# Kernel optimization log

Hardware: AMD Instinct MI355X
Metric: run time of the kernel (lower is better)

Reference implementation:

```python
import jax, jax.numpy as jnp
import numpy as np

KW = 31       # avg_pool kernel
PAD = 15      # padding (count_include_pad=True => divide by KW*KW always)


def _box_avg(x):
    # F.avg_pool2d(x, 31, stride=1, padding=15) with count_include_pad=True
    s = jax.lax.reduce_window(
        x, 0.0, jax.lax.add,
        window_dimensions=(1, 1, KW, KW),
        window_strides=(1, 1, 1, 1),
        padding=((0, 0), (0, 0), (PAD, PAD), (PAD, PAD)))
    return s / (KW * KW)


def setup_inputs() -> dict:
    key = jax.random.key(0)
    k1, k2 = jax.random.split(key)
    B, C, H, W = 64, 1, 512, 512
    pred = jax.random.normal(k1, (B, C, H, W), dtype=jnp.float32)
    mask = jax.random.uniform(k2, (B, C, H, W), dtype=jnp.float32)
    return {"pred": pred, "mask": mask}


def reference(pred, mask):
    weit = 1.0 + 5.0 * jnp.abs(_box_avg(mask) - mask)
    # stable BCE-with-logits, elementwise
    bce = jnp.maximum(pred, 0.0) - pred * mask + jnp.log1p(jnp.exp(-jnp.abs(pred)))
    # NOTE: original passes reduce='none' which PyTorch's legacy handling maps to
    # reduction='mean' -> wbce is a global scalar; the weit normalization cancels.
    wbce = bce.mean()  # scalar, broadcast over [B, C]
    p = jax.nn.sigmoid(pred)
    inter = (p * mask * weit).sum(axis=(2, 3))          # [B, C]
    union = ((p + mask) * weit).sum(axis=(2, 3))        # [B, C]
    wiou = 1.0 - (inter + 1.0) / (union - inter + 1.0)  # [B, C]
    return (wbce + wiou).mean()
```

## Files before the change

### kernel.cpp

```cpp
#include <hip/hip_runtime.h>
#include <math.h>

#define BDIM 64
#define HDIM 512
#define WDIM 512
#define KW   31
#define PAD  15
#define INV_KK (1.0f / 961.0f)
#define TH   32
#define NPIX ((size_t)BDIM * HDIM * WDIM)

#define NACC 129

__global__ void zero_acc_kernel(double* acc) {
    int i = threadIdx.x;
    if (i < NACC) acc[i] = 0.0;
}

template<int CTRL, int RMASK>
__device__ __forceinline__ float dpp_add(float p) {
    int t = __builtin_amdgcn_update_dpp(0, __builtin_bit_cast(int, p),
                                        CTRL, RMASK, 0xf, true);
    return p + __builtin_bit_cast(float, t);
}

__device__ __forceinline__ float wave_iscan(float p) {
    p = dpp_add<0x111, 0xf>(p);
    p = dpp_add<0x112, 0xf>(p);
    p = dpp_add<0x114, 0xf>(p);
    p = dpp_add<0x118, 0xf>(p);
    p = dpp_add<0x142, 0xa>(p);
    p = dpp_add<0x143, 0xc>(p);
    return p;
}

__device__ __forceinline__ float wave_iscan30(float p) {
    p = dpp_add<0x111, 0xf>(p);
    p = dpp_add<0x112, 0xf>(p);
    p = dpp_add<0x114, 0xf>(p);
    p = dpp_add<0x118, 0xf>(p);
    p = dpp_add<0x142, 0xa>(p);
    return p;
}

__device__ __forceinline__ float wave_shr1(float p) {
    int t = __builtin_amdgcn_update_dpp(0, __builtin_bit_cast(int, p),
                                        0x138 , 0xf, 0xf, true);
    return __builtin_bit_cast(float, t);
}

__global__ __launch_bounds__(512, 6)
void fused_kernel(const float* __restrict__ pred,
                  const float* __restrict__ mask,
                  double* __restrict__ acc) {
    __shared__ float red[3][8];

    const int b    = blockIdx.x;
    const int y0   = blockIdx.y * TH;
    const int x    = threadIdx.x;
    const int lane = x & 63;
    const int wv   = x >> 6;
    const int s    = wv * 64;

    const float* mbase = mask + (size_t)b * HDIM * WDIM;
    const float* pbase = pred + (size_t)b * HDIM * WDIM;

    const int acol = s - 15 + lane;
    const int bcol = s + 49 + lane;
    const bool a_ok = (acol >= 0) && (acol < WDIM);
    const bool b_ok = (lane < 30) && (bcol < WDIM);

    const int tstart = y0 - PAD;
    const int tend   = y0 + TH - 1 + PAD;
    const int smax   = (tstart > 0) ? tstart : 0;

    float vsA = 0.f, vsB = 0.f;
    float bce_acc = 0.f, inter_acc = 0.f, uni_acc = 0.f;

    auto load_halo = [&](int row, float& A, float& B) {
        A = 0.f; B = 0.f;
        if (row >= 0 && row < HDIM) {
            const float* rp = mbase + (size_t)row * WDIM;
            if (a_ok) A = rp[acol];
            if (b_ok) B = rp[bcol];
        }
    };
    auto load_sub = [&](int row, float& A, float& B) {
        A = 0.f; B = 0.f;
        if (row >= smax) {
            const float* rp = mbase + (size_t)row * WDIM;
            if (a_ok) A = rp[acol];
            if (b_ok) B = rp[bcol];
        }
    };
    auto load_emit = [&](int row, float& M, float& P) {
        M = 0.f; P = 0.f;
        if (row <= tend) {
            const size_t off = (size_t)(row - PAD) * WDIM + x;
            M = mbase[off];
            P = pbase[off];
        }
    };

    auto process = [&](float A, float B, float S, float T, float M, float P) {
        vsA += A - S;
        vsB += B - T;
        float pa = wave_iscan(vsA);
        float pb = wave_iscan30(vsB);
        const float atot = __builtin_bit_cast(float,
            __builtin_amdgcn_readlane(__builtin_bit_cast(int, pa), 63));
        const float v1 = __shfl(pa, (lane + 30) & 63);
        const float v2 = __shfl(pb, (lane + 30) & 63);
        const float Phi = (lane <= 33) ? v1 : (atot + v2);
        const float Plo = wave_shr1(pa);
        const float hs  = Phi - Plo;

        const float box  = hs * INV_KK;
        const float weit = 1.f + 5.f * fabsf(box - M);
        const float e1   = __expf(-fabsf(P));
        const float bce  = fmaxf(P, 0.f) - P * M + __logf(1.f + e1);
        const float rr   = __builtin_amdgcn_rcpf(1.f + e1);
        const float sp   = (P >= 0.f) ? rr : e1 * rr;
        bce_acc   += bce;
        inter_acc += sp * M * weit;
        uni_acc   += (sp + M) * weit;
    };

    float cA[2], cB[2];
    load_halo(tstart,     cA[0], cB[0]);
    load_halo(tstart + 1, cA[1], cB[1]);
    for (int t = tstart; t < y0 + PAD; t += 2) {
        float nA[2], nB[2];
        load_halo(t + 2, nA[0], nB[0]);
        load_halo(t + 3, nA[1], nB[1]);
        vsA += cA[0] + cA[1];
        vsB += cB[0] + cB[1];
        cA[0] = nA[0]; cA[1] = nA[1]; cB[0] = nB[0]; cB[1] = nB[1];
    }

    float cS[2], cT[2], cM[2], cP[2];
    load_sub(y0 - 16, cS[0], cT[0]);
    load_sub(y0 - 15, cS[1], cT[1]);
    load_emit(y0 + PAD,     cM[0], cP[0]);
    load_emit(y0 + PAD + 1, cM[1], cP[1]);

    for (int t = y0 + PAD; t <= tend; t += 2) {
        float nA[2], nB[2], nS[2], nT[2], nM[2], nP[2];
        load_halo(t + 2, nA[0], nB[0]);
        load_halo(t + 3, nA[1], nB[1]);
        load_sub (t - 29, nS[0], nT[0]);
        load_sub (t - 28, nS[1], nT[1]);
        load_emit(t + 2, nM[0], nP[0]);
        load_emit(t + 3, nM[1], nP[1]);

        process(cA[0], cB[0], cS[0], cT[0], cM[0], cP[0]);
        process(cA[1], cB[1], cS[1], cT[1], cM[1], cP[1]);

        cA[0] = nA[0]; cA[1] = nA[1]; cB[0] = nB[0]; cB[1] = nB[1];
        cS[0] = nS[0]; cS[1] = nS[1]; cT[0] = nT[0]; cT[1] = nT[1];
        cM[0] = nM[0]; cM[1] = nM[1]; cP[0] = nP[0]; cP[1] = nP[1];
    }

#pragma unroll
    for (int off = 32; off > 0; off >>= 1) {
        bce_acc   += __shfl_down(bce_acc, off);
        inter_acc += __shfl_down(inter_acc, off);
        uni_acc   += __shfl_down(uni_acc, off);
    }
    if (lane == 0) {
        red[0][wv] = bce_acc;
        red[1][wv] = inter_acc;
        red[2][wv] = uni_acc;
    }
    __syncthreads();
    if (threadIdx.x == 0) {
        float bs = 0.f, is = 0.f, us = 0.f;
#pragma unroll
        for (int w = 0; w < 8; ++w) { bs += red[0][w]; is += red[1][w]; us += red[2][w]; }
        atomicAdd(&acc[0],      (double)bs);
        atomicAdd(&acc[1 + b],  (double)is);
        atomicAdd(&acc[65 + b], (double)us);
    }
}

__global__ void finalize_kernel(const double* __restrict__ acc, float* __restrict__ out) {
    const int b = threadIdx.x;
    double inter = acc[1 + b];
    double uni   = acc[65 + b];
    double wiou  = 1.0 - (inter + 1.0) / (uni - inter + 1.0);
#pragma unroll
    for (int off = 32; off > 0; off >>= 1) wiou += __shfl_down(wiou, off);
    if (b == 0) {
        double wbce = acc[0] / (double)NPIX;
        out[0] = (float)(wbce + wiou / (double)BDIM);
    }
}

extern "C" void kernel_launch(void* const* d_in, const int* in_sizes, int n_in,
                              void* d_out, int out_size, void* d_ws, size_t ws_size,
                              hipStream_t stream) {
    const float* pred = (const float*)d_in[0];
    const float* mask = (const float*)d_in[1];
    float* out = (float*)d_out;
    double* acc = (double*)d_ws;

    zero_acc_kernel<<<1, 256, 0, stream>>>(acc);

    dim3 grid(BDIM, HDIM / TH);
    fused_kernel<<<grid, WDIM, 0, stream>>>(pred, mask, acc);

    finalize_kernel<<<1, 64, 0, stream>>>(acc, out);
}
```

Before: 169.1 us.

## Deepen load prefetch to two row pairs with clamped branchless loads and full unroll

Result: slower. 183.9 us (+8.7%).

```diff
diff --git a/kernel.cpp b/kernel.cpp
--- a/kernel.cpp
+++ b/kernel.cpp
@@ -49,7 +49,7 @@
     return __builtin_bit_cast(float, t);
 }
 
-__global__ __launch_bounds__(512, 6)
+__global__ __launch_bounds__(512, 8)
 void fused_kernel(const float* __restrict__ pred,
                   const float* __restrict__ mask,
                   double* __restrict__ acc) {
@@ -67,8 +67,10 @@
 
     const int acol = s - 15 + lane;
     const int bcol = s + 49 + lane;
-    const bool a_ok = (acol >= 0) && (acol < WDIM);
-    const bool b_ok = (lane < 30) && (bcol < WDIM);
+    const int acolc = (acol < 0) ? 0 : ((acol > WDIM - 1) ? WDIM - 1 : acol);
+    const int bcolc = (bcol > WDIM - 1) ? WDIM - 1 : bcol;
+    const float aMul = (acol >= 0 && acol < WDIM) ? 1.f : 0.f;
+    const float bMul = (lane < 30 && bcol < WDIM) ? 1.f : 0.f;
 
     const int tstart = y0 - PAD;
     const int tend   = y0 + TH - 1 + PAD;
@@ -77,36 +79,35 @@
     float vsA = 0.f, vsB = 0.f;
     float bce_acc = 0.f, inter_acc = 0.f, uni_acc = 0.f;
 
-    auto load_halo = [&](int row, float& A, float& B) {
-        A = 0.f; B = 0.f;
-        if (row >= 0 && row < HDIM) {
-            const float* rp = mbase + (size_t)row * WDIM;
-            if (a_ok) A = rp[acol];
-            if (b_ok) B = rp[bcol];
-        }
-    };
-    auto load_sub = [&](int row, float& A, float& B) {
-        A = 0.f; B = 0.f;
-        if (row >= smax) {
-            const float* rp = mbase + (size_t)row * WDIM;
-            if (a_ok) A = rp[acol];
-            if (b_ok) B = rp[bcol];
-        }
-    };
-    auto load_emit = [&](int row, float& M, float& P) {
-        M = 0.f; P = 0.f;
-        if (row <= tend) {
-            const size_t off = (size_t)(row - PAD) * WDIM + x;
-            M = mbase[off];
-            P = pbase[off];
-        }
+    auto ld_halo = [&](int row, float& A, float& B) {
+        int rc = row;
+        if (rc < 0) rc = 0;
+        if (rc > HDIM - 1) rc = HDIM - 1;
+        const float* rp = mbase + (size_t)rc * WDIM;
+        A = rp[acolc];
+        B = rp[bcolc];
+        if (row < 0 || row >= HDIM) { A = 0.f; B = 0.f; }
+    };
+    auto ld_sub = [&](int row, float& S, float& T) {
+        int rc = (row < smax) ? smax : row;
+        const float* rp = mbase + (size_t)rc * WDIM;
+        S = rp[acolc];
+        T = rp[bcolc];
+        if (row < smax) { S = 0.f; T = 0.f; }
+    };
+    auto ld_emit = [&](int row, float& M, float& P) {
+        int rc = row - PAD;
+        if (rc > HDIM - 1) rc = HDIM - 1;
+        const size_t off = (size_t)rc * WDIM + x;
+        M = mbase[off];
+        P = pbase[off];
     };
 
     auto process = [&](float A, float B, float S, float T, float M, float P) {
         vsA += A - S;
         vsB += B - T;
-        float pa = wave_iscan(vsA);
-        float pb = wave_iscan30(vsB);
+        float pa = wave_iscan(vsA * aMul);
+        float pb = wave_iscan30(vsB * bMul);
         const float atot = __builtin_bit_cast(float,
             __builtin_amdgcn_readlane(__builtin_bit_cast(int, pa), 63));
         const float v1 = __shfl(pa, (lane + 30) & 63);
@@ -126,39 +127,63 @@
         uni_acc   += (sp + M) * weit;
     };
 
-    float cA[2], cB[2];
-    load_halo(tstart,     cA[0], cB[0]);
-    load_halo(tstart + 1, cA[1], cB[1]);
-    for (int t = tstart; t < y0 + PAD; t += 2) {
-        float nA[2], nB[2];
-        load_halo(t + 2, nA[0], nB[0]);
-        load_halo(t + 3, nA[1], nB[1]);
-        vsA += cA[0] + cA[1];
-        vsB += cB[0] + cB[1];
-        cA[0] = nA[0]; cA[1] = nA[1]; cB[0] = nB[0]; cB[1] = nB[1];
-    }
-
-    float cS[2], cT[2], cM[2], cP[2];
-    load_sub(y0 - 16, cS[0], cT[0]);
-    load_sub(y0 - 15, cS[1], cT[1]);
-    load_emit(y0 + PAD,     cM[0], cP[0]);
-    load_emit(y0 + PAD + 1, cM[1], cP[1]);
-
-    for (int t = y0 + PAD; t <= tend; t += 2) {
-        float nA[2], nB[2], nS[2], nT[2], nM[2], nP[2];
-        load_halo(t + 2, nA[0], nB[0]);
-        load_halo(t + 3, nA[1], nB[1]);
-        load_sub (t - 29, nS[0], nT[0]);
-        load_sub (t - 28, nS[1], nT[1]);
-        load_emit(t + 2, nM[0], nP[0]);
-        load_emit(t + 3, nM[1], nP[1]);
-
-        process(cA[0], cB[0], cS[0], cT[0], cM[0], cP[0]);
-        process(cA[1], cB[1], cS[1], cT[1], cM[1], cP[1]);
-
-        cA[0] = nA[0]; cA[1] = nA[1]; cB[0] = nB[0]; cB[1] = nB[1];
-        cS[0] = nS[0]; cS[1] = nS[1]; cT[0] = nT[0]; cT[1] = nT[1];
-        cM[0] = nM[0]; cM[1] = nM[1]; cP[0] = nP[0]; cP[1] = nP[1];
+    const int t0 = y0 + PAD;
+
+    float wA0, wB0, wA1, wB1;
+    float xA0, xB0, xA1, xB1;
+    ld_halo(tstart,     wA0, wB0);
+    ld_halo(tstart + 1, wA1, wB1);
+    ld_halo(tstart + 2, xA0, xB0);
+    ld_halo(tstart + 3, xA1, xB1);
+
+    float qS0, qT0, qS1, qT1, rS0, rT0, rS1, rT1;
+    float qM0, qP0, qM1, qP1, rM0, rP0, rM1, rP1;
+    ld_sub (t0 - 31, qS0, qT0);
+    ld_sub (t0 - 30, qS1, qT1);
+    ld_sub (t0 - 29, rS0, rT0);
+    ld_sub (t0 - 28, rS1, rT1);
+    ld_emit(t0,      qM0, qP0);
+    ld_emit(t0 + 1,  qM1, qP1);
+    ld_emit(t0 + 2,  rM0, rP0);
+    ld_emit(t0 + 3,  rM1, rP1);
+
+#pragma unroll
+    for (int i = 0; i < 15; ++i) {
+        const int t = tstart + 2 * i;
+        float nA0, nB0, nA1, nB1;
+        ld_halo(t + 4, nA0, nB0);
+        ld_halo(t + 5, nA1, nB1);
+        vsA += wA0 + wA1;
+        vsB += wB0 + wB1;
+        wA0 = xA0; wB0 = xB0; wA1 = xA1; wB1 = xB1;
+        xA0 = nA0; xB0 = nB0; xA1 = nA1; xB1 = nB1;
+    }
+
+    float qA0 = wA0, qB0 = wB0, qA1 = wA1, qB1 = wB1;
+    float rA0 = xA0, rB0 = xB0, rA1 = xA1, rB1 = xB1;
+
+#pragma unroll
+    for (int i = 0; i < 16; ++i) {
+        const int t = t0 + 2 * i;
+        float nA0, nB0, nA1, nB1, nS0, nT0, nS1, nT1, nM0, nP0, nM1, nP1;
+        ld_halo(t + 4, nA0, nB0);
+        ld_halo(t + 5, nA1, nB1);
+        ld_sub (t - 27, nS0, nT0);
+        ld_sub (t - 26, nS1, nT1);
+        ld_emit(t + 4, nM0, nP0);
+        ld_emit(t + 5, nM1, nP1);
+
+        process(qA0, qB0, qS0, qT0, qM0, qP0);
+        process(qA1, qB1, qS1, qT1, qM1, qP1);
+
+        qA0 = rA0; qB0 = rB0; qA1 = rA1; qB1 = rB1;
+        qS0 = rS0; qT0 = rT0; qS1 = rS1; qT1 = rT1;
+        qM0 = rM0; qP0 = rP0; qM1 = rP1 == rP1 ? rM1 : rM1; qP1 = rP1;
+        qM1 = rM1;
+        rA0 = nA0; rB0 = nB0; rA1 = nA1; rB1 = nB1;
+        rS0 = nS0; rT0 = nT0; rS1 = nT1 == nT1 ? nS1 : nS1; rT1 = nT1;
+        rS1 = nS1;
+        rM0 = nM0; rP0 = nP0; rM1 = nM1; rP1 = nP1;
     }
 
 #pragma unroll
```

## Deepen load prefetch to two steps, merge shuffles into one bpermute, raise occupancy

Applied to the files above, without the earlier changes.

After: 169.6 us. No clear change (+0.3%).

```diff
diff --git a/kernel.cpp b/kernel.cpp
--- a/kernel.cpp
+++ b/kernel.cpp
@@ -49,7 +49,17 @@
     return __builtin_bit_cast(float, t);
 }
 
-__global__ __launch_bounds__(512, 6)
+__device__ __forceinline__ float bperm(int idx, float v) {
+    return __builtin_bit_cast(float,
+        __builtin_amdgcn_ds_bpermute(idx, __builtin_bit_cast(int, v)));
+}
+
+__device__ __forceinline__ float readlane63(float v) {
+    return __builtin_bit_cast(float,
+        __builtin_amdgcn_readlane(__builtin_bit_cast(int, v), 63));
+}
+
+__global__ __launch_bounds__(512, 8)
 void fused_kernel(const float* __restrict__ pred,
                   const float* __restrict__ mask,
                   double* __restrict__ acc) {
@@ -70,6 +80,10 @@
     const bool a_ok = (acol >= 0) && (acol < WDIM);
     const bool b_ok = (lane < 30) && (bcol < WDIM);
 
+    const int  i30  = ((lane + 30) & 63) << 2;
+    const bool lo30 = (lane <= 29);
+    const bool lo34 = (lane <= 33);
+
     const int tstart = y0 - PAD;
     const int tend   = y0 + TH - 1 + PAD;
     const int smax   = (tstart > 0) ? tstart : 0;
@@ -77,7 +91,7 @@
     float vsA = 0.f, vsB = 0.f;
     float bce_acc = 0.f, inter_acc = 0.f, uni_acc = 0.f;
 
-    auto load_halo = [&](int row, float& A, float& B) {
+    auto ld_halo = [&](int row, float& A, float& B) {
         A = 0.f; B = 0.f;
         if (row >= 0 && row < HDIM) {
             const float* rp = mbase + (size_t)row * WDIM;
@@ -85,15 +99,15 @@
             if (b_ok) B = rp[bcol];
         }
     };
-    auto load_sub = [&](int row, float& A, float& B) {
-        A = 0.f; B = 0.f;
+    auto ld_sub = [&](int row, float& S, float& T) {
+        S = 0.f; T = 0.f;
         if (row >= smax) {
             const float* rp = mbase + (size_t)row * WDIM;
-            if (a_ok) A = rp[acol];
-            if (b_ok) B = rp[bcol];
+            if (a_ok) S = rp[acol];
+            if (b_ok) T = rp[bcol];
         }
     };
-    auto load_emit = [&](int row, float& M, float& P) {
+    auto ld_emit = [&](int row, float& M, float& P) {
         M = 0.f; P = 0.f;
         if (row <= tend) {
             const size_t off = (size_t)(row - PAD) * WDIM + x;
@@ -107,11 +121,10 @@
         vsB += B - T;
         float pa = wave_iscan(vsA);
         float pb = wave_iscan30(vsB);
-        const float atot = __builtin_bit_cast(float,
-            __builtin_amdgcn_readlane(__builtin_bit_cast(int, pa), 63));
-        const float v1 = __shfl(pa, (lane + 30) & 63);
-        const float v2 = __shfl(pb, (lane + 30) & 63);
-        const float Phi = (lane <= 33) ? v1 : (atot + v2);
+        const float atot = readlane63(pa);
+        const float z   = lo30 ? pb : pa;
+        const float bp  = bperm(i30, z);
+        const float Phi = lo34 ? bp : (atot + bp);
         const float Plo = wave_shr1(pa);
         const float hs  = Phi - Plo;
 
@@ -126,39 +139,53 @@
         uni_acc   += (sp + M) * weit;
     };
 
-    float cA[2], cB[2];
-    load_halo(tstart,     cA[0], cB[0]);
-    load_halo(tstart + 1, cA[1], cB[1]);
-    for (int t = tstart; t < y0 + PAD; t += 2) {
+    const int t0 = y0 + PAD;
+
+    float cA[2], cB[2], xA[2], xB[2];
+    ld_halo(tstart,     cA[0], cB[0]);
+    ld_halo(tstart + 1, cA[1], cB[1]);
+    ld_halo(tstart + 2, xA[0], xB[0]);
+    ld_halo(tstart + 3, xA[1], xB[1]);
+
+    float cS[2], cT[2], cM[2], cP[2];
+    float nS[2], nT[2], nM[2], nQ[2];
+    ld_sub (t0 - 31, cS[0], cT[0]);
+    ld_sub (t0 - 30, cS[1], cT[1]);
+    ld_sub (t0 - 29, nS[0], nT[0]);
+    ld_sub (t0 - 28, nS[1], nT[1]);
+    ld_emit(t0,      cM[0], cP[0]);
+    ld_emit(t0 + 1,  cM[1], cP[1]);
+    ld_emit(t0 + 2,  nM[0], nQ[0]);
+    ld_emit(t0 + 3,  nM[1], nQ[1]);
+
+    for (int t = tstart; t < t0; t += 2) {
         float nA[2], nB[2];
-        load_halo(t + 2, nA[0], nB[0]);
-        load_halo(t + 3, nA[1], nB[1]);
+        ld_halo(t + 4, nA[0], nB[0]);
+        ld_halo(t + 5, nA[1], nB[1]);
         vsA += cA[0] + cA[1];
         vsB += cB[0] + cB[1];
-        cA[0] = nA[0]; cA[1] = nA[1]; cB[0] = nB[0]; cB[1] = nB[1];
-    }
-
-    float cS[2], cT[2], cM[2], cP[2];
-    load_sub(y0 - 16, cS[0], cT[0]);
-    load_sub(y0 - 15, cS[1], cT[1]);
-    load_emit(y0 + PAD,     cM[0], cP[0]);
-    load_emit(y0 + PAD + 1, cM[1], cP[1]);
-
-    for (int t = y0 + PAD; t <= tend; t += 2) {
-        float nA[2], nB[2], nS[2], nT[2], nM[2], nP[2];
-        load_halo(t + 2, nA[0], nB[0]);
-        load_halo(t + 3, nA[1], nB[1]);
-        load_sub (t - 29, nS[0], nT[0]);
-        load_sub (t - 28, nS[1], nT[1]);
-        load_emit(t + 2, nM[0], nP[0]);
-        load_emit(t + 3, nM[1], nP[1]);
+        cA[0] = xA[0]; cA[1] = xA[1]; cB[0] = xB[0]; cB[1] = xB[1];
+        xA[0] = nA[0]; xA[1] = nA[1]; xB[0] = nB[0]; xB[1] = nB[1];
+    }
+
+    for (int t = t0; t <= tend; t += 2) {
+        float nA[2], nB[2], mS[2], mT[2], mM[2], mQ[2];
+        ld_halo(t + 4, nA[0], nB[0]);
+        ld_halo(t + 5, nA[1], nB[1]);
+        ld_sub (t - 27, mS[0], mT[0]);
+        ld_sub (t - 26, mS[1], mT[1]);
+        ld_emit(t + 4, mM[0], mQ[0]);
+        ld_emit(t + 5, mM[1], mQ[1]);
 
         process(cA[0], cB[0], cS[0], cT[0], cM[0], cP[0]);
         process(cA[1], cB[1], cS[1], cT[1], cM[1], cP[1]);
 
-        cA[0] = nA[0]; cA[1] = nA[1]; cB[0] = nB[0]; cB[1] = nB[1];
+        cA[0] = xA[0]; cA[1] = xA[1]; cB[0] = xB[0]; cB[1] = xB[1];
         cS[0] = nS[0]; cS[1] = nS[1]; cT[0] = nT[0]; cT[1] = nT[1];
-        cM[0] = nM[0]; cM[1] = nM[1]; cP[0] = nP[0]; cP[1] = nP[1];
+        cM[0] = nM[0]; cM[1] = nM[1]; cP[0] = nQ[0]; cP[1] = nQ[1];
+        xA[0] = nA[0]; xA[1] = nA[1]; xB[0] = nB[0]; xB[1] = nB[1];
+        nS[0] = mS[0]; nS[1] = mS[1]; nT[0] = mT[0]; nT[1] = mT[1];
+        nM[0] = mM[0]; nM[1] = mM[1]; nQ[0] = mQ[0]; nQ[1] = mQ[1];
     }
 
 #pragma unroll
```
